# Optimization experiments

Hardware: AMD Instinct MI355X
Metric: run time of the kernel (lower is better)

The kernel has to match this reference:

```python
import jax, jax.numpy as jnp
import numpy as np

B, T = 64, 2048
DQ, A, E = 1024, 128, 512
NF, K = 32, 31
PAD = (K - 1) // 2


def setup_inputs() -> dict:
    key = jax.random.key(0)
    ks = jax.random.split(key, 8)
    s = 0.02
    return {
        "query": jax.random.normal(ks[0], (B, 1, DQ), jnp.float32),
        "memory": jax.random.normal(ks[1], (B, T, E), jnp.float32),
        "attention_weights_cat": jax.random.uniform(ks[2], (B, 2, T), jnp.float32),
        "W_query": jax.random.normal(ks[3], (A, DQ), jnp.float32) * s,
        "W_memory": jax.random.normal(ks[4], (A, E), jnp.float32) * s,
        "conv_w": jax.random.normal(ks[5], (NF, 2, K), jnp.float32) * s,
        "W_loc": jax.random.normal(ks[6], (A, NF), jnp.float32) * s,
        "v": jax.random.normal(ks[7], (1, A), jnp.float32) * s,
    }


def reference(query, memory, attention_weights_cat, W_query, W_memory, conv_w, W_loc, v):
    # projected key: [B, T, A]
    key = jnp.einsum("bte,ae->bta", memory, W_memory)
    # projected query: [B, 1, A]
    q = jnp.einsum("bsd,ad->bsa", query, W_query)
    # location features: Conv1d (2 -> NF, same padding, no bias) then linear to A
    loc = jax.lax.conv_general_dilated(
        attention_weights_cat, conv_w,
        window_strides=(1,), padding=[(PAD, PAD)],
        dimension_numbers=("NCH", "OIH", "NCH"))  # [B, NF, T]
    loc = jnp.einsum("bft,af->bta", loc, W_loc)  # [B, T, A]
    # additive energies -> scalar score per position
    energies = jnp.einsum("bta,oa->bto", jnp.tanh(q + key + loc), v)[..., 0]  # [B, T]
    attention_weights = jax.nn.softmax(energies, axis=1)  # [B, T]
    attention_context = jnp.einsum("bt,bte->be", attention_weights, memory)  # [B, E]
    return attention_context, attention_weights
```

## Files before the change

kernel.cpp:

```cpp
#include <hip/hip_runtime.h>
#include <hip/hip_bf16.h>
#include <stdint.h>

#define B_   64
#define T_   2048
#define DQ_  1024
#define A_   128
#define E_   512
#define NF_  32
#define KW_  31
#define PAD_ 15
#define KE_  544

typedef __attribute__((ext_vector_type(8))) short bf16x8;
typedef __attribute__((ext_vector_type(4))) float f32x4;

#define OFF_WCAT 0
#define OFF_Q    139264
#define OFF_EN   172032
#define OFF_ST   696320

__device__ inline ushort f2bf(float f) {
  uint32_t u = __float_as_uint(f);
  u += 0x7fffu + ((u >> 16) & 1u);
  return (ushort)(u >> 16);
}
__device__ inline uint32_t pkbf(float a, float b) {
  uint32_t x = __float_as_uint(a), y = __float_as_uint(b);
  x += 0x7fffu + ((x >> 16) & 1u);
  y += 0x7fffu + ((y >> 16) & 1u);
  return (x >> 16) | (y & 0xffff0000u);
}
__device__ inline float tanh_fast(float x) {
  float cx = fminf(fmaxf(x, -15.f), 15.f);
  float e = __expf(2.f * cx);
  return (e - 1.f) / (e + 1.f);
}

__global__ void prep_wcat(const float* __restrict__ wmem, const float* __restrict__ wloc,
                          ushort* __restrict__ wcat) {
  int a = blockIdx.x, tid = threadIdx.x;
  for (int c = tid; c < E_; c += 256) wcat[a*KE_ + c] = f2bf(wmem[a*E_ + c]);
  if (tid < NF_) wcat[a*KE_ + E_ + tid] = f2bf(wloc[a*NF_ + tid]);
}

__global__ void prep_q(const float* __restrict__ query, const float* __restrict__ wq,
                       float* __restrict__ q) {
  __shared__ float qS[DQ_];
  int b = blockIdx.x, tid = threadIdx.x;
  for (int d = tid; d < DQ_; d += 128) qS[d] = query[b*DQ_ + d];
  __syncthreads();
  const float* wr = wq + (long)tid*DQ_;
  float s = 0.f;
  for (int d = 0; d < DQ_; d += 4) {
    float4 w4 = *(const float4*)(wr + d);
    s = fmaf(qS[d],   w4.x, s); s = fmaf(qS[d+1], w4.y, s);
    s = fmaf(qS[d+2], w4.z, s); s = fmaf(qS[d+3], w4.w, s);
  }
  q[b*A_ + tid] = s;
}

__launch_bounds__(256)
__global__ void energy_kernel(const float* __restrict__ memf, const float* __restrict__ aw,
                              const float* __restrict__ cw, const ushort* __restrict__ wcat,
                              const float* __restrict__ q, const float* __restrict__ vvec,
                              float* __restrict__ energies, float* __restrict__ stats) {
  __shared__ uint4 As4[1024];
  __shared__ uint4 Bs4[1024];
  __shared__ float epS[256];
  __shared__ float awS[2][160];
  __shared__ float cwS[NF_*2*KW_];
  __shared__ float redS[4];
  const int tid  = threadIdx.x;
  const int lane = tid & 63, wid = tid >> 6;
  const int wm = wid >> 1, wn = wid & 1;
  const int fr = lane & 15, fk = lane >> 4;
  const long row0 = (long)blockIdx.x * 128;
  const int b = (int)(row0 >> 11);
  const int t0 = (int)(row0 & (T_-1));

  for (int i = tid; i < 158; i += 256) {
    int g = t0 + i - PAD_;
    bool ok = (g >= 0) && (g < T_);
    awS[0][i] = ok ? aw[(long)b*2*T_ + g]      : 0.f;
    awS[1][i] = ok ? aw[(long)b*2*T_ + T_ + g] : 0.f;
  }
  for (int i = tid; i < NF_*2*KW_; i += 256) cwS[i] = cw[i];

  f32x4 acc[4][4];
  #pragma unroll
  for (int m = 0; m < 4; ++m)
    #pragma unroll
    for (int n = 0; n < 4; ++n) acc[m][n] = (f32x4){0.f,0.f,0.f,0.f};

  for (int kt = 0; kt < 9; ++kt) {
    __syncthreads();
    if (kt < 8) {
      const int k0 = kt*64;
      #pragma unroll
      for (int i = 0; i < 4; ++i) {
        int c = i*256 + tid;
        int r = c >> 3, cl = c & 7;
        const float* src = memf + (row0 + r)*E_ + k0 + cl*8;
        float4 x = *(const float4*)src;
        float4 y = *(const float4*)(src + 4);
        uint4 p = { pkbf(x.x,x.y), pkbf(x.z,x.w), pkbf(y.x,y.y), pkbf(y.z,y.w) };
        As4[r*8 + (cl ^ (r & 7))] = p;
      }
      #pragma unroll
      for (int i = 0; i < 4; ++i) {
        int c = i*256 + tid;
        int r = c >> 3, cd = c & 7;
        int cl = cd ^ (r & 7);
        const ushort* src = wcat + r*KE_ + k0 + cl*8;
        __builtin_amdgcn_global_load_lds((const __attribute__((address_space(1))) void*)src,
                                         (__attribute__((address_space(3))) void*)(Bs4 + c),
                                         16, 0, 0);
      }
    } else {
      #pragma unroll
      for (int i = 0; i < 2; ++i) {
        int c = i*256 + tid;
        int r = c >> 2, cl = c & 3;
        float f[8];
        #pragma unroll
        for (int j = 0; j < 8; ++j) {
          const float* c0 = &cwS[(cl*8 + j)*2*KW_];
          float s = 0.f;
          #pragma unroll
          for (int k = 0; k < KW_; ++k) {
            s = fmaf(awS[0][r + k], c0[k],       s);
            s = fmaf(awS[1][r + k], c0[KW_ + k], s);
          }
          f[j] = s;
        }
        uint4 p = { pkbf(f[0],f[1]), pkbf(f[2],f[3]), pkbf(f[4],f[5]), pkbf(f[6],f[7]) };
        As4[r*8 + (cl ^ (r & 7))] = p;
      }
      #pragma unroll
      for (int i = 0; i < 2; ++i) {
        int c = i*256 + tid;
        int r = c >> 2, cl = c & 3;
        uint4 w = *(const uint4*)(wcat + r*KE_ + E_ + cl*8);
        Bs4[r*8 + (cl ^ (r & 7))] = w;
      }
    }
    __syncthreads();
    const ushort* As = (const ushort*)As4;
    const ushort* Bs = (const ushort*)Bs4;
    const int nkk = (kt < 8) ? 2 : 1;
    for (int kk = 0; kk < nkk; ++kk) {
      bf16x8 af[4], bfr[4];
      const int clk = kk*4 + fk;
      #pragma unroll
      for (int m = 0; m < 4; ++m) {
        int r = wm*64 + m*16 + fr;
        af[m] = *(const bf16x8*)(As + r*64 + (clk ^ (r & 7))*8);
      }
      #pragma unroll
      for (int n = 0; n < 4; ++n) {
        int r = wn*64 + n*16 + fr;
        bfr[n] = *(const bf16x8*)(Bs + r*64 + (clk ^ (r & 7))*8);
      }
      #pragma unroll
      for (int m = 0; m < 4; ++m)
        #pragma unroll
        for (int n = 0; n < 4; ++n)
          acc[m][n] = __builtin_amdgcn_mfma_f32_16x16x32_bf16(af[m], bfr[n], acc[m][n], 0, 0, 0);
    }
  }

  const float* qb = q + b*A_;
  float ep[4][4];
  #pragma unroll
  for (int m = 0; m < 4; ++m)
    #pragma unroll
    for (int r = 0; r < 4; ++r) ep[m][r] = 0.f;
  #pragma unroll
  for (int n = 0; n < 4; ++n) {
    int col = wn*64 + n*16 + fr;
    float qa = qb[col];
    float va = vvec[col];
    #pragma unroll
    for (int m = 0; m < 4; ++m)
      #pragma unroll
      for (int r = 0; r < 4; ++r)
        ep[m][r] = fmaf(va, tanh_fast(acc[m][n][r] + qa), ep[m][r]);
  }
  #pragma unroll
  for (int m = 0; m < 4; ++m)
    #pragma unroll
    for (int r = 0; r < 4; ++r) {
      float v = ep[m][r];
      v += __shfl_xor(v, 1); v += __shfl_xor(v, 2);
      v += __shfl_xor(v, 4); v += __shfl_xor(v, 8);
      ep[m][r] = v;
    }
  if (fr == 0) {
    #pragma unroll
    for (int m = 0; m < 4; ++m)
      #pragma unroll
      for (int r = 0; r < 4; ++r)
        epS[wn*128 + wm*64 + m*16 + fk*4 + r] = ep[m][r];
  }
  __syncthreads();
  float e = -1e30f;
  if (tid < 128) {
    e = epS[tid] + epS[128 + tid];
    energies[row0 + tid] = e;
  }
  float mx = e;
  #pragma unroll
  for (int o = 32; o > 0; o >>= 1) mx = fmaxf(mx, __shfl_xor(mx, o));
  if (lane == 0) redS[wid] = mx;
  __syncthreads();
  mx = fmaxf(fmaxf(redS[0], redS[1]), fmaxf(redS[2], redS[3]));
  float sx = (tid < 128) ? __expf(e - mx) : 0.f;
  #pragma unroll
  for (int o = 32; o > 0; o >>= 1) sx += __shfl_xor(sx, o);
  __syncthreads();
  if (lane == 0) redS[wid] = sx;
  __syncthreads();
  if (tid == 0) {
    stats[2*blockIdx.x]     = mx;
    stats[2*blockIdx.x + 1] = redS[0] + redS[1] + redS[2] + redS[3];
  }
}

__launch_bounds__(256)
__global__ void smctx_kernel(const float* __restrict__ memf, const float* __restrict__ energies,
                             const float* __restrict__ stats, float* __restrict__ outw,
                             float* __restrict__ ctx) {
  __shared__ float wS[128];
  const int blk = blockIdx.x;
  const int b = blk >> 4;
  const int t0 = (blk & 15) * 128;
  const int tid = threadIdx.x;
  float M = -1e30f;
  #pragma unroll
  for (int j = 0; j < 16; ++j) M = fmaxf(M, stats[2*(b*16 + j)]);
  float Z = 0.f;
  #pragma unroll
  for (int j = 0; j < 16; ++j) Z += stats[2*(b*16 + j) + 1] * __expf(stats[2*(b*16 + j)] - M);
  const float invZ = 1.f / Z;
  if (tid < 128) {
    float w = __expf(energies[(long)b*T_ + t0 + tid] - M) * invZ;
    outw[(long)b*T_ + t0 + tid] = w;
    wS[tid] = w;
  }
  __syncthreads();
  const float* mb = memf + ((long)b*T_ + t0)*E_;
  float ax = 0.f, ay = 0.f;
  #pragma unroll 8
  for (int t = 0; t < 128; ++t) {
    float wt = wS[t];
    float2 m2 = *(const float2*)(mb + (long)t*E_ + tid*2);
    ax = fmaf(wt, m2.x, ax);
    ay = fmaf(wt, m2.y, ay);
  }
  atomicAdd(&ctx[b*E_ + tid*2],     ax);
  atomicAdd(&ctx[b*E_ + tid*2 + 1], ay);
}

extern "C" void kernel_launch(void* const* d_in, const int* in_sizes, int n_in,
                              void* d_out, int out_size, void* d_ws, size_t ws_size,
                              hipStream_t stream) {
  const float* query  = (const float*)d_in[0];
  const float* memory = (const float*)d_in[1];
  const float* awcat  = (const float*)d_in[2];
  const float* wq     = (const float*)d_in[3];
  const float* wmem   = (const float*)d_in[4];
  const float* convw  = (const float*)d_in[5];
  const float* wloc   = (const float*)d_in[6];
  const float* vvec   = (const float*)d_in[7];

  char* ws = (char*)d_ws;
  ushort* wcat    = (ushort*)(ws + OFF_WCAT);
  float*  qproj   = (float*)(ws + OFF_Q);
  float*  energies= (float*)(ws + OFF_EN);
  float*  stats   = (float*)(ws + OFF_ST);

  float* ctx  = (float*)d_out;
  float* outw = (float*)d_out + B_*E_;

  hipMemsetAsync(ctx, 0, B_*E_*sizeof(float), stream);
  prep_wcat<<<128, 256, 0, stream>>>(wmem, wloc, wcat);
  prep_q<<<64, 128, 0, stream>>>(query, wq, qproj);
  energy_kernel<<<1024, 256, 0, stream>>>(memory, awcat, convw, wcat, qproj, vvec,
                                          energies, stats);
  smctx_kernel<<<1024, 256, 0, stream>>>(memory, energies, stats, outw, ctx);
}
```

Measured before the change: 534.9 us.

## Split conv into own kernel, load MFMA operands directly from global, halve smctx tiles

The location convolution moves into a separate kernel that writes bf16 features to workspace. The energy GEMM drops its LDS staging and syncs: each wave loads its 32 memory rows and all 128 W columns straight from global into MFMA fragments. The smctx kernel now uses 64-row tiles across twice as many blocks. This removes LDS traffic and barriers, but adds an extra launch and reads W redundantly per wave from global or cache, with uncoalesced-strided fragment loads.

```diff
diff --git a/kernel.cpp b/kernel.cpp
--- a/kernel.cpp
+++ b/kernel.cpp
@@ -19,6 +19,7 @@
 #define OFF_Q    139264
 #define OFF_EN   172032
 #define OFF_ST   696320
+#define OFF_CF   704512
 
 __device__ inline ushort f2bf(float f) {
   uint32_t u = __float_as_uint(f);
@@ -60,166 +61,146 @@
   q[b*A_ + tid] = s;
 }
 
-__launch_bounds__(256)
-__global__ void energy_kernel(const float* __restrict__ memf, const float* __restrict__ aw,
-                              const float* __restrict__ cw, const ushort* __restrict__ wcat,
-                              const float* __restrict__ q, const float* __restrict__ vvec,
-                              float* __restrict__ energies, float* __restrict__ stats) {
-  __shared__ uint4 As4[1024];
-  __shared__ uint4 Bs4[1024];
-  __shared__ float epS[256];
-  __shared__ float awS[2][160];
+__global__ void conv_kernel(const float* __restrict__ aw, const float* __restrict__ cw,
+                            ushort* __restrict__ convf) {
+  __shared__ float awS[2][96];
   __shared__ float cwS[NF_*2*KW_];
-  __shared__ float redS[4];
-  const int tid  = threadIdx.x;
-  const int lane = tid & 63, wid = tid >> 6;
-  const int wm = wid >> 1, wn = wid & 1;
-  const int fr = lane & 15, fk = lane >> 4;
-  const long row0 = (long)blockIdx.x * 128;
-  const int b = (int)(row0 >> 11);
-  const int t0 = (int)(row0 & (T_-1));
-
-  for (int i = tid; i < 158; i += 256) {
+  const int blk = blockIdx.x;
+  const int b = blk >> 5, t0 = (blk & 31) * 64;
+  const int tid = threadIdx.x;
+  const int r = tid >> 2, c = tid & 3;
+  for (int i = tid; i < 94; i += 256) {
     int g = t0 + i - PAD_;
     bool ok = (g >= 0) && (g < T_);
     awS[0][i] = ok ? aw[(long)b*2*T_ + g]      : 0.f;
     awS[1][i] = ok ? aw[(long)b*2*T_ + T_ + g] : 0.f;
   }
   for (int i = tid; i < NF_*2*KW_; i += 256) cwS[i] = cw[i];
-
-  f32x4 acc[4][4];
-  #pragma unroll
-  for (int m = 0; m < 4; ++m)
-    #pragma unroll
-    for (int n = 0; n < 4; ++n) acc[m][n] = (f32x4){0.f,0.f,0.f,0.f};
-
-  for (int kt = 0; kt < 9; ++kt) {
-    __syncthreads();
-    if (kt < 8) {
-      const int k0 = kt*64;
-      #pragma unroll
-      for (int i = 0; i < 4; ++i) {
-        int c = i*256 + tid;
-        int r = c >> 3, cl = c & 7;
-        const float* src = memf + (row0 + r)*E_ + k0 + cl*8;
-        float4 x = *(const float4*)src;
-        float4 y = *(const float4*)(src + 4);
-        uint4 p = { pkbf(x.x,x.y), pkbf(x.z,x.w), pkbf(y.x,y.y), pkbf(y.z,y.w) };
-        As4[r*8 + (cl ^ (r & 7))] = p;
-      }
-      #pragma unroll
-      for (int i = 0; i < 4; ++i) {
-        int c = i*256 + tid;
-        int r = c >> 3, cd = c & 7;
-        int cl = cd ^ (r & 7);
-        const ushort* src = wcat + r*KE_ + k0 + cl*8;
-        __builtin_amdgcn_global_load_lds((const __attribute__((address_space(1))) void*)src,
-                                         (__attribute__((address_space(3))) void*)(Bs4 + c),
-                                         16, 0, 0);
-      }
-    } else {
-      #pragma unroll
-      for (int i = 0; i < 2; ++i) {
-        int c = i*256 + tid;
-        int r = c >> 2, cl = c & 3;
-        float f[8];
+  __syncthreads();
+  float f[8];
+  #pragma unroll
+  for (int j = 0; j < 8; ++j) f[j] = 0.f;
+  #pragma unroll
+  for (int k = 0; k < KW_; ++k) {
+    float a0 = awS[0][r + k], a1 = awS[1][r + k];
+    #pragma unroll
+    for (int j = 0; j < 8; ++j) {
+      const float* c0 = &cwS[(c*8 + j)*2*KW_];
+      f[j] = fmaf(a0, c0[k], f[j]);
+      f[j] = fmaf(a1, c0[KW_ + k], f[j]);
+    }
+  }
+  uint4 p = { pkbf(f[0],f[1]), pkbf(f[2],f[3]), pkbf(f[4],f[5]), pkbf(f[6],f[7]) };
+  uint4* out4 = (uint4*)convf;
+  out4[(long)(b*T_ + t0 + r)*4 + c] = p;
+}
+
+__launch_bounds__(256)
+__global__ void energy_kernel(const float* __restrict__ memf, const ushort* __restrict__ convf,
+                              const ushort* __restrict__ wcat, const float* __restrict__ q,
+                              const float* __restrict__ vvec, float* __restrict__ energies,
+                              float* __restrict__ stats) {
+  __shared__ float epS[128];
+  __shared__ float redS[4];
+  const int tid  = threadIdx.x;
+  const int lane = tid & 63, w = tid >> 6;
+  const int fr = lane & 15, fk = lane >> 4;
+  const long rowB = (long)blockIdx.x * 128;
+  const long row0 = rowB + w*32;
+  const int b = (int)(rowB >> 11);
+
+  f32x4 acc[2][8];
+  #pragma unroll
+  for (int m = 0; m < 2; ++m)
+    #pragma unroll
+    for (int n = 0; n < 8; ++n) acc[m][n] = (f32x4){0.f,0.f,0.f,0.f};
+
+  const float*  a0p = memf + (row0 + fr)*E_;
+  const float*  a1p = memf + (row0 + 16 + fr)*E_;
+  const ushort* bp  = wcat + fr*KE_;
+
+  #pragma unroll 1
+  for (int kt = 0; kt < 8; ++kt) {
+    #pragma unroll
+    for (int kk = 0; kk < 2; ++kk) {
+      const int k = kt*64 + kk*32 + fk*8;
+      float4 x0 = *(const float4*)(a0p + k);
+      float4 y0 = *(const float4*)(a0p + k + 4);
+      float4 x1 = *(const float4*)(a1p + k);
+      float4 y1 = *(const float4*)(a1p + k + 4);
+      bf16x8 am[2];
+      { uint4 p0 = { pkbf(x0.x,x0.y), pkbf(x0.z,x0.w), pkbf(y0.x,y0.y), pkbf(y0.z,y0.w) };
+        uint4 p1 = { pkbf(x1.x,x1.y), pkbf(x1.z,x1.w), pkbf(y1.x,y1.y), pkbf(y1.z,y1.w) };
+        am[0] = *(bf16x8*)&p0; am[1] = *(bf16x8*)&p1; }
+      bf16x8 bn[8];
+      #pragma unroll
+      for (int n = 0; n < 8; ++n)
+        bn[n] = *(const bf16x8*)(bp + n*16*KE_ + k);
+      #pragma unroll
+      for (int m = 0; m < 2; ++m)
         #pragma unroll
-        for (int j = 0; j < 8; ++j) {
-          const float* c0 = &cwS[(cl*8 + j)*2*KW_];
-          float s = 0.f;
-          #pragma unroll
-          for (int k = 0; k < KW_; ++k) {
-            s = fmaf(awS[0][r + k], c0[k],       s);
-            s = fmaf(awS[1][r + k], c0[KW_ + k], s);
-          }
-          f[j] = s;
-        }
-        uint4 p = { pkbf(f[0],f[1]), pkbf(f[2],f[3]), pkbf(f[4],f[5]), pkbf(f[6],f[7]) };
-        As4[r*8 + (cl ^ (r & 7))] = p;
-      }
-      #pragma unroll
-      for (int i = 0; i < 2; ++i) {
-        int c = i*256 + tid;
-        int r = c >> 2, cl = c & 3;
-        uint4 w = *(const uint4*)(wcat + r*KE_ + E_ + cl*8);
-        Bs4[r*8 + (cl ^ (r & 7))] = w;
-      }
+        for (int n = 0; n < 8; ++n)
+          acc[m][n] = __builtin_amdgcn_mfma_f32_16x16x32_bf16(am[m], bn[n], acc[m][n], 0, 0, 0);
     }
-    __syncthreads();
-    const ushort* As = (const ushort*)As4;
-    const ushort* Bs = (const ushort*)Bs4;
-    const int nkk = (kt < 8) ? 2 : 1;
-    for (int kk = 0; kk < nkk; ++kk) {
-      bf16x8 af[4], bfr[4];
-      const int clk = kk*4 + fk;
-      #pragma unroll
-      for (int m = 0; m < 4; ++m) {
-        int r = wm*64 + m*16 + fr;
-        af[m] = *(const bf16x8*)(As + r*64 + (clk ^ (r & 7))*8);
-      }
-      #pragma unroll
-      for (int n = 0; n < 4; ++n) {
-        int r = wn*64 + n*16 + fr;
-        bfr[n] = *(const bf16x8*)(Bs + r*64 + (clk ^ (r & 7))*8);
-      }
-      #pragma unroll
-      for (int m = 0; m < 4; ++m)
-        #pragma unroll
-        for (int n = 0; n < 4; ++n)
-          acc[m][n] = __builtin_amdgcn_mfma_f32_16x16x32_bf16(af[m], bfr[n], acc[m][n], 0, 0, 0);
-    }
+  }
+  {
+    bf16x8 am[2];
+    am[0] = *(const bf16x8*)(convf + (row0 + fr)*NF_      + fk*8);
+    am[1] = *(const bf16x8*)(convf + (row0 + 16 + fr)*NF_ + fk*8);
+    bf16x8 bn[8];
+    #pragma unroll
+    for (int n = 0; n < 8; ++n)
+      bn[n] = *(const bf16x8*)(bp + n*16*KE_ + E_ + fk*8);
+    #pragma unroll
+    for (int m = 0; m < 2; ++m)
+      #pragma unroll
+      for (int n = 0; n < 8; ++n)
+        acc[m][n] = __builtin_amdgcn_mfma_f32_16x16x32_bf16(am[m], bn[n], acc[m][n], 0, 0, 0);
   }
 
   const float* qb = q + b*A_;
-  float ep[4][4];
-  #pragma unroll
-  for (int m = 0; m < 4; ++m)
+  float ep[2][4];
+  #pragma unroll
+  for (int m = 0; m < 2; ++m)
     #pragma unroll
     for (int r = 0; r < 4; ++r) ep[m][r] = 0.f;
   #pragma unroll
-  for (int n = 0; n < 4; ++n) {
-    int col = wn*64 + n*16 + fr;
+  for (int n = 0; n < 8; ++n) {
+    int col = n*16 + fr;
     float qa = qb[col];
     float va = vvec[col];
     #pragma unroll
-    for (int m = 0; m < 4; ++m)
+    for (int m = 0; m < 2; ++m)
       #pragma unroll
       for (int r = 0; r < 4; ++r)
         ep[m][r] = fmaf(va, tanh_fast(acc[m][n][r] + qa), ep[m][r]);
   }
   #pragma unroll
-  for (int m = 0; m < 4; ++m)
+  for (int m = 0; m < 2; ++m)
     #pragma unroll
     for (int r = 0; r < 4; ++r) {
       float v = ep[m][r];
       v += __shfl_xor(v, 1); v += __shfl_xor(v, 2);
       v += __shfl_xor(v, 4); v += __shfl_xor(v, 8);
-      ep[m][r] = v;
+      if (fr == 0) epS[w*32 + m*16 + fk*4 + r] = v;
     }
-  if (fr == 0) {
-    #pragma unroll
-    for (int m = 0; m < 4; ++m)
-      #pragma unroll
-      for (int r = 0; r < 4; ++r)
-        epS[wn*128 + wm*64 + m*16 + fk*4 + r] = ep[m][r];
-  }
   __syncthreads();
   float e = -1e30f;
   if (tid < 128) {
-    e = epS[tid] + epS[128 + tid];
-    energies[row0 + tid] = e;
+    e = epS[tid];
+    energies[rowB + tid] = e;
   }
   float mx = e;
   #pragma unroll
   for (int o = 32; o > 0; o >>= 1) mx = fmaxf(mx, __shfl_xor(mx, o));
-  if (lane == 0) redS[wid] = mx;
+  if (lane == 0) redS[w] = mx;
   __syncthreads();
   mx = fmaxf(fmaxf(redS[0], redS[1]), fmaxf(redS[2], redS[3]));
   float sx = (tid < 128) ? __expf(e - mx) : 0.f;
   #pragma unroll
   for (int o = 32; o > 0; o >>= 1) sx += __shfl_xor(sx, o);
   __syncthreads();
-  if (lane == 0) redS[wid] = sx;
+  if (lane == 0) redS[w] = sx;
   __syncthreads();
   if (tid == 0) {
     stats[2*blockIdx.x]     = mx;
@@ -231,10 +212,10 @@
 __global__ void smctx_kernel(const float* __restrict__ memf, const float* __restrict__ energies,
                              const float* __restrict__ stats, float* __restrict__ outw,
                              float* __restrict__ ctx) {
-  __shared__ float wS[128];
+  __shared__ float wS[64];
   const int blk = blockIdx.x;
-  const int b = blk >> 4;
-  const int t0 = (blk & 15) * 128;
+  const int b = blk >> 5;
+  const int t0 = (blk & 31) * 64;
   const int tid = threadIdx.x;
   float M = -1e30f;
   #pragma unroll
@@ -243,7 +224,7 @@
   #pragma unroll
   for (int j = 0; j < 16; ++j) Z += stats[2*(b*16 + j) + 1] * __expf(stats[2*(b*16 + j)] - M);
   const float invZ = 1.f / Z;
-  if (tid < 128) {
+  if (tid < 64) {
     float w = __expf(energies[(long)b*T_ + t0 + tid] - M) * invZ;
     outw[(long)b*T_ + t0 + tid] = w;
     wS[tid] = w;
@@ -251,8 +232,8 @@
   __syncthreads();
   const float* mb = memf + ((long)b*T_ + t0)*E_;
   float ax = 0.f, ay = 0.f;
-  #pragma unroll 8
-  for (int t = 0; t < 128; ++t) {
+  #pragma unroll 16
+  for (int t = 0; t < 64; ++t) {
     float wt = wS[t];
     float2 m2 = *(const float2*)(mb + (long)t*E_ + tid*2);
     ax = fmaf(wt, m2.x, ax);
@@ -279,6 +260,7 @@
   float*  qproj   = (float*)(ws + OFF_Q);
   float*  energies= (float*)(ws + OFF_EN);
   float*  stats   = (float*)(ws + OFF_ST);
+  ushort* convf   = (ushort*)(ws + OFF_CF);
 
   float* ctx  = (float*)d_out;
   float* outw = (float*)d_out + B_*E_;
@@ -286,7 +268,8 @@
   hipMemsetAsync(ctx, 0, B_*E_*sizeof(float), stream);
   prep_wcat<<<128, 256, 0, stream>>>(wmem, wloc, wcat);
   prep_q<<<64, 128, 0, stream>>>(query, wq, qproj);
-  energy_kernel<<<1024, 256, 0, stream>>>(memory, awcat, convw, wcat, qproj, vvec,
+  conv_kernel<<<2048, 256, 0, stream>>>(awcat, convw, convf);
+  energy_kernel<<<1024, 256, 0, stream>>>(memory, convf, wcat, qproj, vvec,
                                           energies, stats);
-  smctx_kernel<<<1024, 256, 0, stream>>>(memory, energies, stats, outw, ctx);
-}
+  smctx_kernel<<<2048, 256, 0, stream>>>(memory, energies, stats, outw, ctx);
+}
```

Measured after the change: 506.0 us. -5.4%, faster.
